# Performance work log

Hardware: AMD Instinct MI355X
Metric: run time of the kernel (lower is better)

The kernel has to match this reference:

```python
import jax, jax.numpy as jnp
import numpy as np

DIM = 1024
NUM_EXPERTS = 8
TOP_K = 2


def setup_inputs() -> dict:
    key = jax.random.key(0)
    ks = jax.random.split(key, 7)
    s_in = 1.0 / np.sqrt(DIM)
    s_hid = 1.0 / np.sqrt(4 * DIM)
    x = jax.random.normal(ks[0], (2, 2048, DIM), dtype=jnp.float32)
    gate_w = jax.random.normal(ks[1], (DIM, NUM_EXPERTS), dtype=jnp.float32) * s_in
    gate_b = jax.random.normal(ks[2], (NUM_EXPERTS,), dtype=jnp.float32) * 0.01
    w1 = jax.random.normal(ks[3], (NUM_EXPERTS, DIM, 4 * DIM), dtype=jnp.float32) * s_in
    b1 = jax.random.normal(ks[4], (NUM_EXPERTS, 4 * DIM), dtype=jnp.float32) * 0.01
    w2 = jax.random.normal(ks[5], (NUM_EXPERTS, 4 * DIM, DIM), dtype=jnp.float32) * s_hid
    b2 = jax.random.normal(ks[6], (NUM_EXPERTS, DIM), dtype=jnp.float32) * 0.01
    return {"x": x, "gate_w": gate_w, "gate_b": gate_b, "w1": w1, "b1": b1, "w2": w2, "b2": b2}


def reference(x, gate_w, gate_b, w1, b1, w2, b2):
    # Faithful to the torch module in EVAL mode (no routing noise).
    # Quirks reproduced: (1) gather of expert inputs degenerates to flat_x
    # (all top_k copies identical); (2) softmax-normalized gates are dead code
    # (never applied); (3) the per-expert masked assignment overwrites all
    # TOP_K. Net: out = TOP_K * FFN_{max(topk_idx)}(x).
    B, N, C = x.shape
    flat_x = x.reshape(-1, C)                      # [T, C]
    logits = flat_x @ gate_w + gate_b              # [T, E]
    _, topk_idx = jax.lax.top_k(logits, TOP_K)     # [T, k]
    e_star = jnp.max(topk_idx, axis=-1)            # [T] last-overwriting expert
    out = jnp.zeros_like(flat_x)
    for i in range(NUM_EXPERTS):                   # fixed small expert loop
        h = jax.nn.gelu(flat_x @ w1[i] + b1[i], approximate=False)  # exact GELU (torch default)
        y = h @ w2[i] + b2[i]                      # [T, C]
        out = jnp.where((e_star == i)[:, None], y, out)
    return (TOP_K * out).reshape(B, N, C)
```

## Files before the change

kernel.cpp:

```cpp
#include <hip/hip_runtime.h>
#include <hip/hip_bf16.h>
#include <hip/hip_fp16.h>

#define T_TOKENS 4096
#define DIMC 1024
#define HID 4096
#define NE 8

typedef _Float16 f16;
typedef _Float16 f16x8 __attribute__((ext_vector_type(8)));
typedef _Float16 f16x4 __attribute__((ext_vector_type(4)));
typedef float f32x4 __attribute__((ext_vector_type(4)));

__device__ __forceinline__ void gload_lds16(const f16* g, f16* l) {
    __builtin_amdgcn_global_load_lds(
        (const __attribute__((address_space(1))) void*)g,
        (__attribute__((address_space(3))) void*)l, 16, 0, 0);
}

__device__ __forceinline__ void gating_body(
    int bid, int tid, const float* __restrict__ x, const float* __restrict__ gw,
    const float* __restrict__ gb, int* __restrict__ counts,
    int* __restrict__ list, int* __restrict__ eidx)
{
    const int wave = tid >> 6;
    const int lane = tid & 63;
    const int t = bid * 4 + wave;

    const float* xr = x + (size_t)t * DIMC;
    float acc[NE];
#pragma unroll
    for (int e = 0; e < NE; ++e) acc[e] = 0.f;
    for (int i = 0; i < DIMC / 64; ++i) {
        const int k = i * 64 + lane;
        const float xv = xr[k];
        const float* g = gw + (size_t)k * NE;
#pragma unroll
        for (int e = 0; e < NE; ++e) acc[e] = fmaf(xv, g[e], acc[e]);
    }
#pragma unroll
    for (int off = 32; off >= 1; off >>= 1) {
#pragma unroll
        for (int e = 0; e < NE; ++e) acc[e] += __shfl_xor(acc[e], off, 64);
    }
    if (lane == 0) {
        float lg[NE];
#pragma unroll
        for (int e = 0; e < NE; ++e) lg[e] = acc[e] + gb[e];
        int i1 = 0; float v1 = lg[0];
#pragma unroll
        for (int e = 1; e < NE; ++e) { if (lg[e] > v1) { v1 = lg[e]; i1 = e; } }
        int i2 = -1; float v2 = -3.4e38f;
#pragma unroll
        for (int e = 0; e < NE; ++e) {
            if (e == i1) continue;
            if (lg[e] > v2) { v2 = lg[e]; i2 = e; }
        }
        const int es = (i1 > i2) ? i1 : i2;
        const int pos = atomicAdd(&counts[es], 1);
        list[es * T_TOKENS + pos] = t;
        eidx[t] = es;
    }
}

__global__ __launch_bounds__(256) void gating_kernel(
    const float* __restrict__ x, const float* __restrict__ gw,
    const float* __restrict__ gb, int* __restrict__ counts,
    int* __restrict__ list, int* __restrict__ eidx)
{
    gating_body(blockIdx.x, threadIdx.x, x, gw, gb, counts, list, eidx);
}

__global__ __launch_bounds__(256) void xconvert(const float* __restrict__ x,
                                                f16* __restrict__ xh)
{
    const size_t i = ((size_t)blockIdx.x * 256 + threadIdx.x) * 8;
    const float4 a = *(const float4*)(x + i);
    const float4 b = *(const float4*)(x + i + 4);
    f16x8 v;
    v[0] = (f16)a.x; v[1] = (f16)a.y; v[2] = (f16)a.z; v[3] = (f16)a.w;
    v[4] = (f16)b.x; v[5] = (f16)b.y; v[6] = (f16)b.z; v[7] = (f16)b.w;
    *(f16x8*)(xh + i) = v;
}

__device__ __forceinline__ void wconv_tile(
    const float* __restrict__ W, f16* __restrict__ Wt, int K, int N,
    int bx, int by, int bz, int t, f16* Lt)
{
    const int n0 = bx * 64;
    const int k0 = by * 64;
    const float* Ws = W + (size_t)bz * K * N;
    const int no = (t & 15) * 4;
    const int kr = t >> 4;
#pragma unroll
    for (int p = 0; p < 4; ++p) {
        const int k = kr + p * 16;
        const float4 v = *(const float4*)(Ws + (size_t)(k0 + k) * N + n0 + no);
        Lt[(no + 0) * 72 + k] = (f16)v.x;
        Lt[(no + 1) * 72 + k] = (f16)v.y;
        Lt[(no + 2) * 72 + k] = (f16)v.z;
        Lt[(no + 3) * 72 + k] = (f16)v.w;
    }
    __syncthreads();
    const int n = t >> 2;
    const int ko = (t & 3) * 16;
    const f16x8 a = *(const f16x8*)&Lt[n * 72 + ko];
    const f16x8 b = *(const f16x8*)&Lt[n * 72 + ko + 8];
    f16* dst = Wt + ((size_t)bz * N + n0 + n) * K + k0 + ko;
    *(f16x8*)(dst) = a;
    *(f16x8*)(dst + 8) = b;
}

__global__ __launch_bounds__(256) void wconvert(const float* __restrict__ W,
                                                f16* __restrict__ Wt,
                                                int K, int N)
{
    __shared__ f16 Lt[64 * 72];
    wconv_tile(W, Wt, K, N, blockIdx.x, blockIdx.y, blockIdx.z, threadIdx.x, Lt);
}

__global__ __launch_bounds__(512) void gemm1_wc2(
    const f16* __restrict__ A, const f16* __restrict__ Bt,
    const float* __restrict__ w2, f16* __restrict__ w2t,
    const int* __restrict__ counts, const int* __restrict__ list,
    f16* __restrict__ Pout)
{
    __shared__ __align__(16) char smem[25088];
    const int tid = threadIdx.x;
    const int zz  = blockIdx.z;

    if (zz >= 16) {
        const int s = blockIdx.x + blockIdx.y * 16 + (zz - 16) * 512;
        const int h = tid >> 8;
        const int t = s * 2 + h;
        const int bx = t & 15;
        const int by = (t >> 4) & 63;
        const int bz = t >> 10;
        f16* Lt = (f16*)smem + h * (64 * 72);
        wconv_tile(w2, w2t, HID, DIMC, bx, by, bz, tid & 255, Lt);
        return;
    }

    constexpr int KB   = DIMC;
    constexpr int NTOT = HID;
    constexpr int NKT  = 16;

    const int e   = zz >> 1;
    const int ks  = zz & 1;
    const int kk0 = ks * 512;
    const int m0  = blockIdx.y * 128;
    const int n0  = blockIdx.x * 256;
    const int cnt = counts[e];
    if (m0 >= cnt) return;

    f16* As = (f16*)smem;
    f16* Bs = (f16*)(smem + 8192);
    int* rows = (int*)(smem + 8192 + 16384);

    if (tid < 128) rows[tid] = (m0 + tid < cnt) ? list[e * T_TOKENS + m0 + tid] : -1;
    __syncthreads();

    const int lane = tid & 63;
    const int wv   = tid >> 6;
    const int wr   = wv >> 2;
    const int wc   = wv & 3;

    const int lrow4 = lane >> 2;
    const int lslot = lane & 3;

    const int arow = wv * 16 + lrow4;
    int tokA = rows[arow]; if (tokA < 0) tokA = 0;
    const int achunk = lslot ^ (((arow >> 2) ^ arow) & 3);
    const f16* asrc = A + (size_t)tokA * KB + kk0 + achunk * 8;
    f16* adst = As + (wv * 16) * 32;

    const f16* bsrc[2];
    f16* bdst[2];
#pragma unroll
    for (int j = 0; j < 2; ++j) {
        const int brow = wv * 32 + j * 16 + lrow4;
        const int bchunk = lslot ^ (((brow >> 2) ^ brow) & 3);
        bsrc[j] = Bt + ((size_t)e * NTOT + n0 + brow) * KB + kk0 + bchunk * 8;
        bdst[j] = Bs + (wv * 32 + j * 16) * 32;
    }

    f32x4 acc[4][4];
#pragma unroll
    for (int mi = 0; mi < 4; ++mi)
#pragma unroll
        for (int ni = 0; ni < 4; ++ni) acc[mi][ni] = f32x4{0.f, 0.f, 0.f, 0.f};

    for (int kt = 0; kt < NKT; ++kt) {
        const int ko = kt * 32;
        __syncthreads();
        gload_lds16(asrc + ko, adst);
        gload_lds16(bsrc[0] + ko, bdst[0]);
        gload_lds16(bsrc[1] + ko, bdst[1]);
        __syncthreads();
        {
            f16x8 af[4], bf[4];
            const int slot = lane >> 4;
#pragma unroll
            for (int mi = 0; mi < 4; ++mi) {
                const int row = wr * 64 + mi * 16 + (lane & 15);
                const int kb  = (slot ^ (((row >> 2) ^ row) & 3)) << 4;
                af[mi] = *(const f16x8*)((const char*)As + row * 64 + kb);
            }
#pragma unroll
            for (int ni = 0; ni < 4; ++ni) {
                const int n  = wc * 64 + ni * 16 + (lane & 15);
                const int kb = (slot ^ (((n >> 2) ^ n) & 3)) << 4;
                bf[ni] = *(const f16x8*)((const char*)Bs + n * 64 + kb);
            }
#pragma unroll
            for (int mi = 0; mi < 4; ++mi)
#pragma unroll
                for (int ni = 0; ni < 4; ++ni)
                    acc[mi][ni] = __builtin_amdgcn_mfma_f32_16x16x32_f16(
                        af[mi], bf[ni], acc[mi][ni], 0, 0, 0);
        }
    }

#pragma unroll
    for (int ni = 0; ni < 4; ++ni) {
        const int gc = n0 + wc * 64 + ni * 16 + (lane & 15);
#pragma unroll
        for (int mi = 0; mi < 4; ++mi) {
#pragma unroll
            for (int r = 0; r < 4; ++r) {
                const int lrow = wr * 64 + mi * 16 + (lane >> 4) * 4 + r;
                const int tok = rows[lrow];
                if (tok < 0) continue;
                Pout[((size_t)ks * T_TOKENS + tok) * HID + gc] =
                    (f16)acc[mi][ni][r];
            }
        }
    }
}

__global__ __launch_bounds__(512) void ffn_gemm9b(
    const f16* __restrict__ A, const f16* __restrict__ Bt,
    const int* __restrict__ counts, const int* __restrict__ list,
    f16* __restrict__ Pout)
{
    constexpr int KB   = HID;
    constexpr int NTOT = DIMC;
    constexpr int NKT  = 16;

    const int zz  = blockIdx.z;
    const int e   = zz >> 3;
    const int ks  = zz & 7;
    const int kk0 = ks * 512;
    const int m0  = blockIdx.y * 128;
    const int n0  = blockIdx.x * 256;
    const int cnt = counts[e];
    if (m0 >= cnt) return;

    __shared__ __align__(16) f16 As[128 * 32];
    __shared__ __align__(16) f16 Bs[256 * 32];
    __shared__ int rows[128];

    const int tid = threadIdx.x;
    if (tid < 128) rows[tid] = (m0 + tid < cnt) ? list[e * T_TOKENS + m0 + tid] : -1;
    __syncthreads();

    const int lane = tid & 63;
    const int wv   = tid >> 6;
    const int wr   = wv >> 2;
    const int wc   = wv & 3;

    const int lrow4 = lane >> 2;
    const int lslot = lane & 3;

    const int arow = wv * 16 + lrow4;
    int tokA = rows[arow]; if (tokA < 0) tokA = 0;
    const int achunk = lslot ^ (((arow >> 2) ^ arow) & 3);
    const f16* asrc = A + (size_t)tokA * KB + kk0 + achunk * 8;
    f16* adst = As + (wv * 16) * 32;

    const f16* bsrc[2];
    f16* bdst[2];
#pragma unroll
    for (int j = 0; j < 2; ++j) {
        const int brow = wv * 32 + j * 16 + lrow4;
        const int bchunk = lslot ^ (((brow >> 2) ^ brow) & 3);
        bsrc[j] = Bt + ((size_t)e * NTOT + n0 + brow) * KB + kk0 + bchunk * 8;
        bdst[j] = Bs + (wv * 32 + j * 16) * 32;
    }

    f32x4 acc[4][4];
#pragma unroll
    for (int mi = 0; mi < 4; ++mi)
#pragma unroll
        for (int ni = 0; ni < 4; ++ni) acc[mi][ni] = f32x4{0.f, 0.f, 0.f, 0.f};

    for (int kt = 0; kt < NKT; ++kt) {
        const int ko = kt * 32;
        __syncthreads();
        gload_lds16(asrc + ko, adst);
        gload_lds16(bsrc[0] + ko, bdst[0]);
        gload_lds16(bsrc[1] + ko, bdst[1]);
        __syncthreads();
        {
            f16x8 af[4], bf[4];
            const int slot = lane >> 4;
#pragma unroll
            for (int mi = 0; mi < 4; ++mi) {
                const int row = wr * 64 + mi * 16 + (lane & 15);
                const int kb  = (slot ^ (((row >> 2) ^ row) & 3)) << 4;
                af[mi] = *(const f16x8*)((const char*)As + row * 64 + kb);
            }
#pragma unroll
            for (int ni = 0; ni < 4; ++ni) {
                const int n  = wc * 64 + ni * 16 + (lane & 15);
                const int kb = (slot ^ (((n >> 2) ^ n) & 3)) << 4;
                bf[ni] = *(const f16x8*)((const char*)Bs + n * 64 + kb);
            }
#pragma unroll
            for (int mi = 0; mi < 4; ++mi)
#pragma unroll
                for (int ni = 0; ni < 4; ++ni)
                    acc[mi][ni] = __builtin_amdgcn_mfma_f32_16x16x32_f16(
                        af[mi], bf[ni], acc[mi][ni], 0, 0, 0);
        }
    }

#pragma unroll
    for (int ni = 0; ni < 4; ++ni) {
        const int gc = n0 + wc * 64 + ni * 16 + (lane & 15);
#pragma unroll
        for (int mi = 0; mi < 4; ++mi) {
#pragma unroll
            for (int r = 0; r < 4; ++r) {
                const int lrow = wr * 64 + mi * 16 + (lane >> 4) * 4 + r;
                const int tok = rows[lrow];
                if (tok < 0) continue;
                Pout[((size_t)ks * T_TOKENS + tok) * DIMC + gc] =
                    (f16)acc[mi][ni][r];
            }
        }
    }
}

__global__ __launch_bounds__(256) void gelu_combine(
    const f16* __restrict__ Hp, const float* __restrict__ b1,
    const int* __restrict__ eidx, f16* __restrict__ H)
{
    const size_t i = ((size_t)blockIdx.x * 256 + threadIdx.x) * 8;
    const int t = (int)(i >> 12);
    const int c = (int)(i & (HID - 1));
    const int e = eidx[t];
    const f16x8 a = *(const f16x8*)(Hp + i);
    const f16x8 b = *(const f16x8*)(Hp + (size_t)T_TOKENS * HID + i);
    const float4 ba = *(const float4*)(b1 + (size_t)e * HID + c);
    const float4 bb = *(const float4*)(b1 + (size_t)e * HID + c + 4);
    const float bj[8] = {ba.x, ba.y, ba.z, ba.w, bb.x, bb.y, bb.z, bb.w};
    f16x8 o;
#pragma unroll
    for (int j = 0; j < 8; ++j) {
        const float v = (float)a[j] + (float)b[j] + bj[j];
        o[j] = (f16)(0.5f * v * (1.f + erff(v * 0.70710678118f)));
    }
    *(f16x8*)(H + i) = o;
}

__global__ __launch_bounds__(256) void reduce8(
    const f16* __restrict__ p8, const float* __restrict__ b2,
    const int* __restrict__ eidx, float* __restrict__ out)
{
    constexpr size_t SL = (size_t)T_TOKENS * DIMC;
    const size_t i = ((size_t)blockIdx.x * 256 + threadIdx.x) * 8;
    const int t = (int)(i >> 10);
    const int c = (int)(i & (DIMC - 1));
    const int e = eidx[t];
    float s[8] = {0.f, 0.f, 0.f, 0.f, 0.f, 0.f, 0.f, 0.f};
#pragma unroll
    for (int ks = 0; ks < 8; ++ks) {
        const f16x8 v = *(const f16x8*)(p8 + (size_t)ks * SL + i);
#pragma unroll
        for (int j = 0; j < 8; ++j) s[j] += (float)v[j];
    }
    const float4 ba = *(const float4*)(b2 + (size_t)e * DIMC + c);
    const float4 bb = *(const float4*)(b2 + (size_t)e * DIMC + c + 4);
    const float bj[8] = {ba.x, ba.y, ba.z, ba.w, bb.x, bb.y, bb.z, bb.w};
    float4 o0, o1;
    o0.x = 2.f * (s[0] + bj[0]); o0.y = 2.f * (s[1] + bj[1]);
    o0.z = 2.f * (s[2] + bj[2]); o0.w = 2.f * (s[3] + bj[3]);
    o1.x = 2.f * (s[4] + bj[4]); o1.y = 2.f * (s[5] + bj[5]);
    o1.z = 2.f * (s[6] + bj[6]); o1.w = 2.f * (s[7] + bj[7]);
    *(float4*)(out + i) = o0;
    *(float4*)(out + i + 4) = o1;
}

template <bool FIRST>
__global__ __launch_bounds__(256) void ffn_gemm_fb(
    const float* __restrict__ x, const f16* __restrict__ Hin,
    const float* __restrict__ w1, const float* __restrict__ b1,
    const float* __restrict__ w2, const float* __restrict__ b2,
    const int* __restrict__ counts, const int* __restrict__ list,
    f16* __restrict__ Hout, float* __restrict__ out)
{
    constexpr int K = FIRST ? DIMC : HID;
    constexpr int N = FIRST ? HID : DIMC;
    constexpr int LDT = 40;

    const int e  = blockIdx.z;
    const int m0 = blockIdx.y * 128;
    const int n0 = blockIdx.x * 128;
    const int cnt = counts[e];
    if (m0 >= cnt) return;

    __shared__ f16 Ab[128 * LDT];
    __shared__ f16 Bb[128 * LDT];
    __shared__ int rows[128];

    const int tid = threadIdx.x;
    if (tid < 128) {
        const int p = m0 + tid;
        rows[tid] = (p < cnt) ? list[e * T_TOKENS + p] : -1;
    }
    __syncthreads();

    const int lane = tid & 63;
    const int wv = tid >> 6;
    const int wr = wv >> 1, wc = wv & 1;

    f32x4 acc[4][4];
#pragma unroll
    for (int mi = 0; mi < 4; ++mi)
#pragma unroll
        for (int ni = 0; ni < 4; ++ni) acc[mi][ni] = f32x4{0.f, 0.f, 0.f, 0.f};

    const float* Bsrc = (FIRST ? w1 : w2) + (size_t)e * K * N;

    for (int kk = 0; kk < K; kk += 32) {
        __syncthreads();
        {
            const int r  = tid >> 3;
            const int ko = (tid & 7) * 4;
#pragma unroll
            for (int p = 0; p < 4; ++p) {
                const int row = p * 32 + r;
                const int tok = rows[row];
                f16x4 hv;
                if (FIRST) {
                    float4 v;
                    if (tok >= 0) v = *(const float4*)(x + (size_t)tok * K + kk + ko);
                    else          v = make_float4(0.f, 0.f, 0.f, 0.f);
                    hv[0] = (f16)v.x; hv[1] = (f16)v.y; hv[2] = (f16)v.z; hv[3] = (f16)v.w;
                } else {
                    if (tok >= 0) hv = *(const f16x4*)(Hin + (size_t)tok * K + kk + ko);
                    else { hv[0] = (f16)0.f; hv[1] = (f16)0.f; hv[2] = (f16)0.f; hv[3] = (f16)0.f; }
                }
                *(f16x4*)&Ab[row * LDT + ko] = hv;
            }
        }
        {
            const int kb = tid >> 5;
            const int no = (tid & 31) * 4;
#pragma unroll
            for (int p = 0; p < 4; ++p) {
                const int k = p * 8 + kb;
                const float4 v = *(const float4*)(Bsrc + (size_t)(kk + k) * N + n0 + no);
                f16 h[4];
                h[0] = (f16)v.x; h[1] = (f16)v.y; h[2] = (f16)v.z; h[3] = (f16)v.w;
#pragma unroll
                for (int i = 0; i < 4; ++i) {
                    const int n = no + i;
                    const int chunk = (k >> 3) ^ ((n >> 2) & 3);
                    Bb[n * LDT + chunk * 8 + (k & 7)] = h[i];
                }
            }
        }
        __syncthreads();
        f16x8 af[4], bf[4];
#pragma unroll
        for (int mi = 0; mi < 4; ++mi) {
            const int row = wr * 64 + mi * 16 + (lane & 15);
            af[mi] = *(const f16x8*)&Ab[row * LDT + (lane >> 4) * 8];
        }
#pragma unroll
        for (int ni = 0; ni < 4; ++ni) {
            const int n = wc * 64 + ni * 16 + (lane & 15);
            const int chunk = (lane >> 4) ^ ((n >> 2) & 3);
            bf[ni] = *(const f16x8*)&Bb[n * LDT + chunk * 8];
        }
#pragma unroll
        for (int mi = 0; mi < 4; ++mi)
#pragma unroll
            for (int ni = 0; ni < 4; ++ni)
                acc[mi][ni] = __builtin_amdgcn_mfma_f32_16x16x32_f16(
                    af[mi], bf[ni], acc[mi][ni], 0, 0, 0);
    }

#pragma unroll
    for (int ni = 0; ni < 4; ++ni) {
        const int gc = n0 + wc * 64 + ni * 16 + (lane & 15);
        const float bias = FIRST ? b1[(size_t)e * HID + gc]
                                 : b2[(size_t)e * DIMC + gc];
#pragma unroll
        for (int mi = 0; mi < 4; ++mi) {
#pragma unroll
            for (int r = 0; r < 4; ++r) {
                const int lrow = wr * 64 + mi * 16 + (lane >> 4) * 4 + r;
                const int tok = rows[lrow];
                if (tok < 0) continue;
                const float v = acc[mi][ni][r] + bias;
                if (FIRST) {
                    const float g = 0.5f * v * (1.f + erff(v * 0.70710678118f));
                    Hout[(size_t)tok * HID + gc] = (f16)g;
                } else {
                    out[(size_t)tok * DIMC + gc] = 2.f * v;
                }
            }
        }
    }
}

extern "C" void kernel_launch(void* const* d_in, const int* in_sizes, int n_in,
                              void* d_out, int out_size, void* d_ws, size_t ws_size,
                              hipStream_t stream)
{
    const float* x   = (const float*)d_in[0];
    const float* gw  = (const float*)d_in[1];
    const float* gb  = (const float*)d_in[2];
    const float* w1  = (const float*)d_in[3];
    const float* b1  = (const float*)d_in[4];
    const float* w2  = (const float*)d_in[5];
    const float* b2  = (const float*)d_in[6];
    float* out = (float*)d_out;

    const size_t MB = 1 << 20;
    const size_t need_p = 233 * MB;

    if (ws_size >= need_p) {
        int* counts = (int*)d_ws;
        int* list   = (int*)((char*)d_ws + 1024);
        int* eidx   = (int*)((char*)d_ws + 512 * 1024);
        f16* xh     = (f16*)((char*)d_ws + 1 * MB);
        f16* H      = (f16*)((char*)d_ws + 9 * MB);
        f16* w1t    = (f16*)((char*)d_ws + 41 * MB);
        f16* w2t    = (f16*)((char*)d_ws + 105 * MB);
        f16* Hp     = (f16*)((char*)d_ws + 169 * MB);
        f16* p8     = (f16*)((char*)d_ws + 169 * MB);

        hipMemsetAsync(counts, 0, 1024, stream);

        gating_kernel<<<T_TOKENS / 4, 256, 0, stream>>>(x, gw, gb, counts, list, eidx);
        xconvert<<<(T_TOKENS * DIMC) / (256 * 8), 256, 0, stream>>>(x, xh);
        wconvert<<<dim3(HID / 64, DIMC / 64, NE), 256, 0, stream>>>(w1, w1t, DIMC, HID);

        gemm1_wc2<<<dim3(16, 32, 24), 512, 0, stream>>>(
            xh, w1t, w2, w2t, counts, list, Hp);

        gelu_combine<<<(T_TOKENS * HID) / (256 * 8), 256, 0, stream>>>(Hp, b1, eidx, H);

        ffn_gemm9b<<<dim3(DIMC / 256, T_TOKENS / 128, NE * 8), 512, 0, stream>>>(
            H, w2t, counts, list, p8);

        reduce8<<<(T_TOKENS * DIMC) / (256 * 8), 256, 0, stream>>>(p8, b2, eidx, out);
        return;
    }

    const size_t need_fb = (size_t)(1 << 18) + (size_t)T_TOKENS * HID * sizeof(f16);
    if (ws_size < need_fb) return;

    int* counts = (int*)d_ws;
    int* list   = (int*)((char*)d_ws + 1024);
    int* eidx   = (int*)((char*)d_ws + 160 * 1024);
    f16* H      = (f16*)((char*)d_ws + (1 << 18));

    hipMemsetAsync(d_ws, 0, 1024, stream);
    gating_kernel<<<T_TOKENS / 4, 256, 0, stream>>>(x, gw, gb, counts, list, eidx);
    ffn_gemm_fb<true><<<dim3(HID / 128, T_TOKENS / 128, NE), 256, 0, stream>>>(
        x, (const f16*)nullptr, w1, b1, w2, b2, counts, list, H, out);
    ffn_gemm_fb<false><<<dim3(DIMC / 128, T_TOKENS / 128, NE), 256, 0, stream>>>(
        x, (const f16*)H, w1, b1, w2, b2, counts, list, H, out);
}
```

Measured before the change: 323.5 us.

## Fuse bias and GELU into first GEMM epilogue, drop its split-K

```diff
diff --git a/kernel.cpp b/kernel.cpp
--- a/kernel.cpp
+++ b/kernel.cpp
@@ -121,16 +121,16 @@
 
 __global__ __launch_bounds__(512) void gemm1_wc2(
     const f16* __restrict__ A, const f16* __restrict__ Bt,
-    const float* __restrict__ w2, f16* __restrict__ w2t,
-    const int* __restrict__ counts, const int* __restrict__ list,
-    f16* __restrict__ Pout)
+    const float* __restrict__ b1, const float* __restrict__ w2,
+    f16* __restrict__ w2t, const int* __restrict__ counts,
+    const int* __restrict__ list, f16* __restrict__ H)
 {
     __shared__ __align__(16) char smem[25088];
     const int tid = threadIdx.x;
     const int zz  = blockIdx.z;
 
-    if (zz >= 16) {
-        const int s = blockIdx.x + blockIdx.y * 16 + (zz - 16) * 512;
+    if (zz >= 8) {
+        const int s = blockIdx.x + blockIdx.y * 16 + (zz - 8) * 512;
         const int h = tid >> 8;
         const int t = s * 2 + h;
         const int bx = t & 15;
@@ -143,11 +143,9 @@
 
     constexpr int KB   = DIMC;
     constexpr int NTOT = HID;
-    constexpr int NKT  = 16;
-
-    const int e   = zz >> 1;
-    const int ks  = zz & 1;
-    const int kk0 = ks * 512;
+    constexpr int NKT  = 32;
+
+    const int e   = zz;
     const int m0  = blockIdx.y * 128;
     const int n0  = blockIdx.x * 256;
     const int cnt = counts[e];
@@ -171,7 +169,7 @@
     const int arow = wv * 16 + lrow4;
     int tokA = rows[arow]; if (tokA < 0) tokA = 0;
     const int achunk = lslot ^ (((arow >> 2) ^ arow) & 3);
-    const f16* asrc = A + (size_t)tokA * KB + kk0 + achunk * 8;
+    const f16* asrc = A + (size_t)tokA * KB + achunk * 8;
     f16* adst = As + (wv * 16) * 32;
 
     const f16* bsrc[2];
@@ -180,7 +178,7 @@
     for (int j = 0; j < 2; ++j) {
         const int brow = wv * 32 + j * 16 + lrow4;
         const int bchunk = lslot ^ (((brow >> 2) ^ brow) & 3);
-        bsrc[j] = Bt + ((size_t)e * NTOT + n0 + brow) * KB + kk0 + bchunk * 8;
+        bsrc[j] = Bt + ((size_t)e * NTOT + n0 + brow) * KB + bchunk * 8;
         bdst[j] = Bs + (wv * 32 + j * 16) * 32;
     }
 
@@ -224,6 +222,7 @@
 #pragma unroll
     for (int ni = 0; ni < 4; ++ni) {
         const int gc = n0 + wc * 64 + ni * 16 + (lane & 15);
+        const float bv = b1[(size_t)e * HID + gc];
 #pragma unroll
         for (int mi = 0; mi < 4; ++mi) {
 #pragma unroll
@@ -231,8 +230,9 @@
                 const int lrow = wr * 64 + mi * 16 + (lane >> 4) * 4 + r;
                 const int tok = rows[lrow];
                 if (tok < 0) continue;
-                Pout[((size_t)ks * T_TOKENS + tok) * HID + gc] =
-                    (f16)acc[mi][ni][r];
+                const float v = acc[mi][ni][r] + bv;
+                const float g = 0.5f * v * (1.f + erff(v * 0.70710678118f));
+                H[(size_t)tok * HID + gc] = (f16)g;
             }
         }
     }
@@ -340,28 +340,6 @@
             }
         }
     }
-}
-
-__global__ __launch_bounds__(256) void gelu_combine(
-    const f16* __restrict__ Hp, const float* __restrict__ b1,
-    const int* __restrict__ eidx, f16* __restrict__ H)
-{
-    const size_t i = ((size_t)blockIdx.x * 256 + threadIdx.x) * 8;
-    const int t = (int)(i >> 12);
-    const int c = (int)(i & (HID - 1));
-    const int e = eidx[t];
-    const f16x8 a = *(const f16x8*)(Hp + i);
-    const f16x8 b = *(const f16x8*)(Hp + (size_t)T_TOKENS * HID + i);
-    const float4 ba = *(const float4*)(b1 + (size_t)e * HID + c);
-    const float4 bb = *(const float4*)(b1 + (size_t)e * HID + c + 4);
-    const float bj[8] = {ba.x, ba.y, ba.z, ba.w, bb.x, bb.y, bb.z, bb.w};
-    f16x8 o;
-#pragma unroll
-    for (int j = 0; j < 8; ++j) {
-        const float v = (float)a[j] + (float)b[j] + bj[j];
-        o[j] = (f16)(0.5f * v * (1.f + erff(v * 0.70710678118f)));
-    }
-    *(f16x8*)(H + i) = o;
 }
 
 __global__ __launch_bounds__(256) void reduce8(
@@ -541,7 +519,6 @@
         f16* H      = (f16*)((char*)d_ws + 9 * MB);
         f16* w1t    = (f16*)((char*)d_ws + 41 * MB);
         f16* w2t    = (f16*)((char*)d_ws + 105 * MB);
-        f16* Hp     = (f16*)((char*)d_ws + 169 * MB);
         f16* p8     = (f16*)((char*)d_ws + 169 * MB);
 
         hipMemsetAsync(counts, 0, 1024, stream);
@@ -550,10 +527,8 @@
         xconvert<<<(T_TOKENS * DIMC) / (256 * 8), 256, 0, stream>>>(x, xh);
         wconvert<<<dim3(HID / 64, DIMC / 64, NE), 256, 0, stream>>>(w1, w1t, DIMC, HID);
 
-        gemm1_wc2<<<dim3(16, 32, 24), 512, 0, stream>>>(
-            xh, w1t, w2, w2t, counts, list, Hp);
-
-        gelu_combine<<<(T_TOKENS * HID) / (256 * 8), 256, 0, stream>>>(Hp, b1, eidx, H);
+        gemm1_wc2<<<dim3(16, 32, 16), 512, 0, stream>>>(
+            xh, w1t, b1, w2, w2t, counts, list, H);
 
         ffn_gemm9b<<<dim3(DIMC / 256, T_TOKENS / 128, NE * 8), 512, 0, stream>>>(
             H, w2t, counts, list, p8);
```

Measured after the change: 322.4 us. Within noise of the previous version (-0.3%).
